# Performance work log

Measured on AMD Instinct MI355X. Metric: run time of the kernel, lower is better.

The kernel has to match this reference:

```python
import jax, jax.numpy as jnp
import numpy as np

SIZE = 1024
N_ITER = 10
TEMP = 0.125


def setup_inputs() -> dict:
    key = jax.random.key(0)
    k1, k2 = jax.random.split(key)
    x = jax.random.normal(k1, (8, 4096, SIZE), dtype=jnp.float32)
    # weight init: identity + small gaussian noise (matches torch init)
    weight = jnp.eye(SIZE, dtype=jnp.float32) + jax.random.normal(k2, (SIZE, SIZE), dtype=jnp.float32) * 1e-05
    return {"x": x, "weight": weight}


def _sinkhorn_project(weight):
    # log-space Sinkhorn normalization: n_iter steps of symmetric row/col
    # logsumexp subtraction, then exponentiate.
    log_P = weight / TEMP
    for _ in range(N_ITER):
        r_sum = jax.nn.logsumexp(log_P, axis=-1, keepdims=True)  # [size,1]
        c_sum = jax.nn.logsumexp(log_P, axis=-2, keepdims=True)  # [1,size]
        log_P = log_P - 0.5 * (r_sum + c_sum)
    return jnp.exp(log_P)


def reference(x, weight):
    W = _sinkhorn_project(weight)          # [size, size]
    # F.linear(x, W) == x @ W.T
    return jnp.einsum('bsd,od->bso', x, W)
```

## Files before the change

### kernel.cpp

```cpp
#include <hip/hip_runtime.h>
#include <hip/hip_bf16.h>


typedef __attribute__((ext_vector_type(8))) short short8;
typedef __attribute__((ext_vector_type(4))) float f32x4;

__device__ inline unsigned int pk2(float a, float b) {
  __hip_bfloat162 h = __float22bfloat162_rn(make_float2(a, b));
  union { __hip_bfloat162 h; unsigned int u; } cv;
  cv.h = h;
  return cv.u;
}

__global__ void sinkhorn_step(const float* __restrict__ w,
                              const float* __restrict__ Rin,
                              const float* __restrict__ Cin,
                              float* __restrict__ Rout,
                              float* __restrict__ Cout,
                              int first) {
  __shared__ float red[4];
  const int tid = threadIdx.x;
  const int b = blockIdx.x;
  const int lane = tid & 63, wv = tid >> 6;
  if (b < 1024) {
    const int j = tid * 4;
    float4 v = *(const float4*)(w + (size_t)b * 1024 + j);
    float4 cv = make_float4(0.f, 0.f, 0.f, 0.f);
    if (!first) cv = *(const float4*)(Cin + j);
    float s = __expf(8.f * v.x - 0.5f * cv.x) + __expf(8.f * v.y - 0.5f * cv.y)
            + __expf(8.f * v.z - 0.5f * cv.z) + __expf(8.f * v.w - 0.5f * cv.w);
    #pragma unroll
    for (int off = 32; off > 0; off >>= 1) s += __shfl_down(s, off);
    if (lane == 0) red[wv] = s;
    __syncthreads();
    if (tid == 0) {
      float t = red[0] + red[1] + red[2] + red[3];
      Rout[b] = (first ? 0.f : 0.5f * Rin[b]) + __logf(t);
    }
  } else {
    const int c = b - 1024;
    const int j = ((c & 7) << 7) + (c >> 3);
    const int i0 = tid * 4;
    const float* wp = w + (size_t)i0 * 1024 + j;
    float4 rv = make_float4(0.f, 0.f, 0.f, 0.f);
    if (!first) rv = *(const float4*)(Rin + i0);
    float s = __expf(8.f * wp[0]    - 0.5f * rv.x)
            + __expf(8.f * wp[1024] - 0.5f * rv.y)
            + __expf(8.f * wp[2048] - 0.5f * rv.z)
            + __expf(8.f * wp[3072] - 0.5f * rv.w);
    #pragma unroll
    for (int off = 32; off > 0; off >>= 1) s += __shfl_down(s, off);
    if (lane == 0) red[wv] = s;
    __syncthreads();
    if (tid == 0) {
      float t = red[0] + red[1] + red[2] + red[3];
      Cout[j] = (first ? 0.f : 0.5f * Cin[j]) + __logf(t);
    }
  }
}

__global__ void make_w(const float* __restrict__ w, const float* __restrict__ R,
                       const float* __restrict__ C, unsigned short* __restrict__ Wb) {
  const int i = blockIdx.x;
  const int j = threadIdx.x * 4;
  const float r = 0.5f * R[i];
  float4 v = *(const float4*)(w + (size_t)i * 1024 + j);
  float4 cv = *(const float4*)(C + j);
  unsigned int o[2];
  o[0] = pk2(__expf(8.f * v.x - r - 0.5f * cv.x), __expf(8.f * v.y - r - 0.5f * cv.y));
  o[1] = pk2(__expf(8.f * v.z - r - 0.5f * cv.z), __expf(8.f * v.w - r - 0.5f * cv.w));
  *(uint2*)(Wb + (size_t)i * 1024 + j) = *(uint2*)o;
}

__device__ inline void swizzle_mn(int id, int& m0, int& n0) {
  m0 = ((id & 7) + ((id >> 6) << 3)) << 7;
  n0 = ((id >> 3) & 7) << 7;
}

__global__ __launch_bounds__(256) void gemm_a(const float* __restrict__ X,
                                              const unsigned short* __restrict__ Wb,
                                              float* __restrict__ out) {
  __shared__ unsigned short As[128 * 32];
  __shared__ unsigned short Bs[128 * 32];
  const int tid = threadIdx.x;
  const int lane = tid & 63, wave = tid >> 6;
  const int wm = wave >> 1, wn = wave & 1;
  int m0, n0;
  swizzle_mn(blockIdx.x, m0, n0);

  f32x4 acc[4][4] = {};
  const int sr = tid >> 1, sk = (tid & 1) * 16;
  const float* Xrow = X + (size_t)(m0 + sr) * 1024 + sk;

  for (int k0 = 0; k0 < 1024; k0 += 32) {
    #pragma unroll
    for (int is = 0; is < 2; ++is) {
      int idx = is * 256 + tid;
      const unsigned short* g = Wb + (size_t)(n0 + (idx >> 2)) * 1024 + k0 + (idx & 3) * 8;
      unsigned short* l = Bs + (is * 256 + wave * 64) * 8;
      __builtin_amdgcn_global_load_lds(
          (const __attribute__((address_space(1))) unsigned int*)g,
          (__attribute__((address_space(3))) unsigned int*)l, 16, 0, 0);
    }
    float4 va0 = *(const float4*)(Xrow + k0);
    float4 va1 = *(const float4*)(Xrow + k0 + 4);
    float4 va2 = *(const float4*)(Xrow + k0 + 8);
    float4 va3 = *(const float4*)(Xrow + k0 + 12);
    unsigned int pk[8];
    pk[0] = pk2(va0.x, va0.y); pk[1] = pk2(va0.z, va0.w);
    pk[2] = pk2(va1.x, va1.y); pk[3] = pk2(va1.z, va1.w);
    pk[4] = pk2(va2.x, va2.y); pk[5] = pk2(va2.z, va2.w);
    pk[6] = pk2(va3.x, va3.y); pk[7] = pk2(va3.z, va3.w);
    *(uint4*)(As + sr * 32 + sk)     = *(uint4*)(pk);
    *(uint4*)(As + sr * 32 + sk + 8) = *(uint4*)(pk + 4);

    __syncthreads();

    const int kq = (lane >> 4) * 8;
    const int fr = lane & 15;
    short8 af[4], bf[4];
    #pragma unroll
    for (int t = 0; t < 4; ++t)
      af[t] = *(const short8*)(As + (wm * 64 + t * 16 + fr) * 32 + kq);
    #pragma unroll
    for (int t = 0; t < 4; ++t)
      bf[t] = *(const short8*)(Bs + (wn * 64 + t * 16 + fr) * 32 + kq);
    #pragma unroll
    for (int mt = 0; mt < 4; ++mt)
      #pragma unroll
      for (int nt = 0; nt < 4; ++nt)
        acc[mt][nt] = __builtin_amdgcn_mfma_f32_16x16x32_bf16(af[mt], bf[nt], acc[mt][nt], 0, 0, 0);

    __syncthreads();
  }

  const int crow0 = m0 + wm * 64 + (lane >> 4) * 4;
  const int ccol0 = n0 + wn * 64 + (lane & 15);
  #pragma unroll
  for (int mt = 0; mt < 4; ++mt)
    #pragma unroll
    for (int nt = 0; nt < 4; ++nt)
      #pragma unroll
      for (int r = 0; r < 4; ++r)
        out[(size_t)(crow0 + mt * 16 + r) * 1024 + ccol0 + nt * 16] = acc[mt][nt][r];
}

__global__ __launch_bounds__(256) void gemm_b(const float* __restrict__ X,
                                              const float* __restrict__ w,
                                              const float* __restrict__ R,
                                              const float* __restrict__ C,
                                              float* __restrict__ out) {
  __shared__ unsigned short As[128 * 32];
  __shared__ unsigned short Bs[128 * 32];
  const int tid = threadIdx.x;
  const int lane = tid & 63, wave = tid >> 6;
  const int wm = wave >> 1, wn = wave & 1;
  int m0, n0;
  swizzle_mn(blockIdx.x, m0, n0);

  f32x4 acc[4][4] = {};
  const int sr = tid >> 1, sk = (tid & 1) * 16;
  const float* Xrow = X + (size_t)(m0 + sr) * 1024 + sk;
  const float* Wrow = w + (size_t)(n0 + sr) * 1024 + sk;
  const float rpot = 0.5f * R[n0 + sr];

  for (int k0 = 0; k0 < 1024; k0 += 32) {
    float4 vb0 = *(const float4*)(Wrow + k0);
    float4 vb1 = *(const float4*)(Wrow + k0 + 4);
    float4 vb2 = *(const float4*)(Wrow + k0 + 8);
    float4 vb3 = *(const float4*)(Wrow + k0 + 12);
    float4 vc0 = *(const float4*)(C + k0 + sk);
    float4 vc1 = *(const float4*)(C + k0 + sk + 4);
    float4 vc2 = *(const float4*)(C + k0 + sk + 8);
    float4 vc3 = *(const float4*)(C + k0 + sk + 12);
    unsigned int pb[8];
    pb[0] = pk2(__expf(8.f * vb0.x - rpot - 0.5f * vc0.x), __expf(8.f * vb0.y - rpot - 0.5f * vc0.y));
    pb[1] = pk2(__expf(8.f * vb0.z - rpot - 0.5f * vc0.z), __expf(8.f * vb0.w - rpot - 0.5f * vc0.w));
    pb[2] = pk2(__expf(8.f * vb1.x - rpot - 0.5f * vc1.x), __expf(8.f * vb1.y - rpot - 0.5f * vc1.y));
    pb[3] = pk2(__expf(8.f * vb1.z - rpot - 0.5f * vc1.z), __expf(8.f * vb1.w - rpot - 0.5f * vc1.w));
    pb[4] = pk2(__expf(8.f * vb2.x - rpot - 0.5f * vc2.x), __expf(8.f * vb2.y - rpot - 0.5f * vc2.y));
    pb[5] = pk2(__expf(8.f * vb2.z - rpot - 0.5f * vc2.z), __expf(8.f * vb2.w - rpot - 0.5f * vc2.w));
    pb[6] = pk2(__expf(8.f * vb3.x - rpot - 0.5f * vc3.x), __expf(8.f * vb3.y - rpot - 0.5f * vc3.y));
    pb[7] = pk2(__expf(8.f * vb3.z - rpot - 0.5f * vc3.z), __expf(8.f * vb3.w - rpot - 0.5f * vc3.w));
    float4 va0 = *(const float4*)(Xrow + k0);
    float4 va1 = *(const float4*)(Xrow + k0 + 4);
    float4 va2 = *(const float4*)(Xrow + k0 + 8);
    float4 va3 = *(const float4*)(Xrow + k0 + 12);
    unsigned int pa[8];
    pa[0] = pk2(va0.x, va0.y); pa[1] = pk2(va0.z, va0.w);
    pa[2] = pk2(va1.x, va1.y); pa[3] = pk2(va1.z, va1.w);
    pa[4] = pk2(va2.x, va2.y); pa[5] = pk2(va2.z, va2.w);
    pa[6] = pk2(va3.x, va3.y); pa[7] = pk2(va3.z, va3.w);

    *(uint4*)(Bs + sr * 32 + sk)     = *(uint4*)(pb);
    *(uint4*)(Bs + sr * 32 + sk + 8) = *(uint4*)(pb + 4);
    *(uint4*)(As + sr * 32 + sk)     = *(uint4*)(pa);
    *(uint4*)(As + sr * 32 + sk + 8) = *(uint4*)(pa + 4);

    __syncthreads();

    const int kq = (lane >> 4) * 8;
    const int fr = lane & 15;
    short8 af[4], bf[4];
    #pragma unroll
    for (int t = 0; t < 4; ++t)
      af[t] = *(const short8*)(As + (wm * 64 + t * 16 + fr) * 32 + kq);
    #pragma unroll
    for (int t = 0; t < 4; ++t)
      bf[t] = *(const short8*)(Bs + (wn * 64 + t * 16 + fr) * 32 + kq);
    #pragma unroll
    for (int mt = 0; mt < 4; ++mt)
      #pragma unroll
      for (int nt = 0; nt < 4; ++nt)
        acc[mt][nt] = __builtin_amdgcn_mfma_f32_16x16x32_bf16(af[mt], bf[nt], acc[mt][nt], 0, 0, 0);

    __syncthreads();
  }

  const int crow0 = m0 + wm * 64 + (lane >> 4) * 4;
  const int ccol0 = n0 + wn * 64 + (lane & 15);
  #pragma unroll
  for (int mt = 0; mt < 4; ++mt)
    #pragma unroll
    for (int nt = 0; nt < 4; ++nt)
      #pragma unroll
      for (int r = 0; r < 4; ++r)
        out[(size_t)(crow0 + mt * 16 + r) * 1024 + ccol0 + nt * 16] = acc[mt][nt][r];
}

extern "C" void kernel_launch(void* const* d_in, const int* in_sizes, int n_in,
                              void* d_out, int out_size, void* d_ws, size_t ws_size,
                              hipStream_t stream) {
  const float* x = (const float*)d_in[0];
  const float* weight = (const float*)d_in[1];
  float* out = (float*)d_out;

  float* R0 = (float*)d_ws;
  float* C0 = R0 + 1024;
  float* R1 = C0 + 1024;
  float* C1 = R1 + 1024;
  unsigned short* Wb = (unsigned short*)(C1 + 1024);
  const size_t need_a = 16 * 1024 + 2 * 1024 * 1024;

  for (int t = 0; t < 10; ++t) {
    const float *Ri, *Ci;
    float *Ro, *Co;
    if ((t & 1) == 0) { Ri = R0; Ci = C0; Ro = R1; Co = C1; }
    else              { Ri = R1; Ci = C1; Ro = R0; Co = C0; }
    sinkhorn_step<<<2048, 256, 0, stream>>>(weight, Ri, Ci, Ro, Co, (t == 0) ? 1 : 0);
  }

  if (ws_size >= need_a) {
    make_w<<<1024, 256, 0, stream>>>(weight, R0, C0, Wb);
    gemm_a<<<2048, 256, 0, stream>>>(x, Wb, out);
  } else {
    gemm_b<<<2048, 256, 0, stream>>>(x, weight, R0, C0, out);
  }
}
```

Baseline: 394.0 us.

## Fuse Sinkhorn iterations into one cooperative kernel with grid barriers

Replaces the ten separate sinkhorn_step launches and the make_w launch with a single cooperative kernel of 256 blocks. Each block keeps its slice of exp(8w) in registers, both a row slice and a column slice, and iterates using multiplicative scaling vectors u and v, exchanged through global buffers and a hierarchical atomic grid barrier. This removes repeated launch overhead and repeated re-reading and re-exponentiating of the weight matrix on every iteration. The kernel then writes the bf16 projected weight directly for gemm_a. The trade-off is dependence on cooperative launch and on spin barriers, and it works in the linear domain instead of log space, which could lose precision.

```diff
diff --git a/kernel.cpp b/kernel.cpp
--- a/kernel.cpp
+++ b/kernel.cpp
@@ -10,6 +10,151 @@
   union { __hip_bfloat162 h; unsigned int u; } cv;
   cv.h = h;
   return cv.u;
+}
+
+__device__ __forceinline__ void gbarrier(int* bar, int it) {
+  __syncthreads();
+  if (threadIdx.x == 0) {
+    __threadfence();
+    int* subc = bar + it * 16 + (blockIdx.x & 15);
+    int a = __hip_atomic_fetch_add(subc, 1, __ATOMIC_ACQ_REL, __HIP_MEMORY_SCOPE_AGENT);
+    if (a == 15)
+      __hip_atomic_fetch_add(bar + 160 + it, 1, __ATOMIC_ACQ_REL, __HIP_MEMORY_SCOPE_AGENT);
+    int spins = 0;
+    while (__hip_atomic_load(bar + 160 + it, __ATOMIC_ACQUIRE, __HIP_MEMORY_SCOPE_AGENT) < 16) {
+      __builtin_amdgcn_s_sleep(8);
+      if (++spins > (1 << 22)) break;
+    }
+    __threadfence();
+  }
+  __syncthreads();
+}
+
+__global__ __launch_bounds__(256, 1) void sinkhorn_fused(
+    const float* __restrict__ w,
+    int* __restrict__ bar,
+    float* __restrict__ ubuf,
+    float* __restrict__ vbuf,
+    unsigned short* __restrict__ Wb) {
+  __shared__ float uL[1024];
+  __shared__ float vL[1024];
+  __shared__ float redC[4][4];
+  const int k = blockIdx.x;
+  const int t = threadIdx.x;
+  const int l = t & 63, wv = t >> 6;
+  const int row = 4 * k + wv;
+
+  float er[16];
+  {
+    const float* rp = w + (size_t)row * 1024 + l * 16;
+    #pragma unroll
+    for (int q = 0; q < 4; ++q) {
+      float4 v4 = *(const float4*)(rp + q * 4);
+      er[q * 4 + 0] = __expf(8.f * v4.x);
+      er[q * 4 + 1] = __expf(8.f * v4.y);
+      er[q * 4 + 2] = __expf(8.f * v4.z);
+      er[q * 4 + 3] = __expf(8.f * v4.w);
+    }
+  }
+  float ecs[4][4];
+  {
+    #pragma unroll
+    for (int q = 0; q < 4; ++q) {
+      float4 v4 = *(const float4*)(w + (size_t)(4 * t + q) * 1024 + 4 * k);
+      ecs[q][0] = __expf(8.f * v4.x);
+      ecs[q][1] = __expf(8.f * v4.y);
+      ecs[q][2] = __expf(8.f * v4.z);
+      ecs[q][3] = __expf(8.f * v4.w);
+    }
+  }
+
+  float vold = 1.f;
+  float uold = 1.f;
+
+  for (int it = 0; it < 10; ++it) {
+    const int rsl = it & 1;
+    const int wsl = (it + 1) & 1;
+    float ul[16], vv[4];
+    if (it == 0) {
+      #pragma unroll
+      for (int q = 0; q < 16; ++q) ul[q] = 1.f;
+      vv[0] = vv[1] = vv[2] = vv[3] = 1.f;
+    } else {
+      {
+        float4 uu = *(const float4*)(ubuf + rsl * 1024 + t * 4);
+        float4 vx = *(const float4*)(vbuf + rsl * 1024 + t * 4);
+        int cp = t ^ ((t >> 3) & 7);
+        *(float4*)(uL + cp * 4) = uu;
+        *(float4*)(vL + t * 4) = vx;
+      }
+      __syncthreads();
+      #pragma unroll
+      for (int q = 0; q < 4; ++q) {
+        int c = l * 4 + q;
+        int cp = c ^ ((c >> 3) & 7);
+        float4 u4 = *(const float4*)(uL + cp * 4);
+        ul[q * 4 + 0] = u4.x; ul[q * 4 + 1] = u4.y;
+        ul[q * 4 + 2] = u4.z; ul[q * 4 + 3] = u4.w;
+      }
+      float4 v4 = *(const float4*)(vL + t * 4);
+      vv[0] = v4.x; vv[1] = v4.y; vv[2] = v4.z; vv[3] = v4.w;
+    }
+
+    float rs = 0.f;
+    #pragma unroll
+    for (int q = 0; q < 16; ++q) rs += er[q] * ul[q];
+    #pragma unroll
+    for (int off = 32; off > 0; off >>= 1) rs += __shfl_down(rs, off);
+
+    float cs0 = 0.f, cs1 = 0.f, cs2 = 0.f, cs3 = 0.f;
+    #pragma unroll
+    for (int q = 0; q < 4; ++q) {
+      cs0 += ecs[q][0] * vv[q]; cs1 += ecs[q][1] * vv[q];
+      cs2 += ecs[q][2] * vv[q]; cs3 += ecs[q][3] * vv[q];
+    }
+    #pragma unroll
+    for (int off = 32; off > 0; off >>= 1) {
+      cs0 += __shfl_down(cs0, off); cs1 += __shfl_down(cs1, off);
+      cs2 += __shfl_down(cs2, off); cs3 += __shfl_down(cs3, off);
+    }
+    if (l == 0) {
+      redC[wv][0] = cs0; redC[wv][1] = cs1;
+      redC[wv][2] = cs2; redC[wv][3] = cs3;
+      vold = sqrtf(vold) * rsqrtf(rs);
+      vbuf[wsl * 1024 + row] = vold;
+    }
+    __syncthreads();
+    if (wv == 0 && l < 4) {
+      float tot = redC[0][l] + redC[1][l] + redC[2][l] + redC[3][l];
+      uold = sqrtf(uold) * rsqrtf(tot);
+      ubuf[wsl * 1024 + 4 * k + l] = uold;
+    }
+    gbarrier(bar, it);
+  }
+
+  {
+    float4 uu = *(const float4*)(ubuf + t * 4);
+    int cp = t ^ ((t >> 3) & 7);
+    *(float4*)(uL + cp * 4) = uu;
+  }
+  __syncthreads();
+  const float vfin = __shfl(vold, 0);
+  unsigned int o[8];
+  #pragma unroll
+  for (int q = 0; q < 4; ++q) {
+    int c = l * 4 + q;
+    int cp = c ^ ((c >> 3) & 7);
+    float4 u4 = *(const float4*)(uL + cp * 4);
+    float p0 = er[q * 4 + 0] * vfin * u4.x;
+    float p1 = er[q * 4 + 1] * vfin * u4.y;
+    float p2 = er[q * 4 + 2] * vfin * u4.z;
+    float p3 = er[q * 4 + 3] * vfin * u4.w;
+    o[q * 2 + 0] = pk2(p0, p1);
+    o[q * 2 + 1] = pk2(p2, p3);
+  }
+  unsigned short* wp = Wb + (size_t)row * 1024 + l * 16;
+  *(uint4*)(wp) = *(uint4*)(o);
+  *(uint4*)(wp + 8) = *(uint4*)(o + 4);
 }
 
 __global__ void sinkhorn_step(const float* __restrict__ w,
@@ -235,11 +380,39 @@
   const float* weight = (const float*)d_in[1];
   float* out = (float*)d_out;
 
+  int* bar = (int*)d_ws;
+  float* ubuf = (float*)d_ws + 256;
+  float* vbuf = ubuf + 2048;
+  unsigned short* WbP = (unsigned short*)(vbuf + 2048);
+  const size_t need_p = 1024 + 16 * 1024 + 2 * 1024 * 1024;
+
+  if (ws_size >= need_p) {
+    hipError_t e0 = hipMemsetAsync(bar, 0, 1024, stream);
+    if (e0 == hipSuccess) {
+      const float* warg = weight;
+      int* barArg = bar;
+      float* uArg = ubuf; float* vArg = vbuf;
+      unsigned short* WbArg = WbP;
+      void* args[5] = {(void*)&warg, (void*)&barArg, (void*)&uArg,
+                       (void*)&vArg, (void*)&WbArg};
+      hipError_t ce = hipLaunchCooperativeKernel((const void*)sinkhorn_fused,
+                                                 dim3(256), dim3(256), args, 0,
+                                                 stream);
+      if (ce == hipSuccess) {
+        gemm_a<<<2048, 256, 0, stream>>>(x, WbP, out);
+        return;
+      }
+      (void)hipGetLastError();
+    } else {
+      (void)hipGetLastError();
+    }
+  }
+
   float* R0 = (float*)d_ws;
   float* C0 = R0 + 1024;
   float* R1 = C0 + 1024;
   float* C1 = R1 + 1024;
-  unsigned short* Wb = (unsigned short*)(C1 + 1024);
+  unsigned short* Wb2 = (unsigned short*)(C1 + 1024);
   const size_t need_a = 16 * 1024 + 2 * 1024 * 1024;
 
   for (int t = 0; t < 10; ++t) {
@@ -249,10 +422,9 @@
     else              { Ri = R1; Ci = C1; Ro = R0; Co = C0; }
     sinkhorn_step<<<2048, 256, 0, stream>>>(weight, Ri, Ci, Ro, Co, (t == 0) ? 1 : 0);
   }
-
   if (ws_size >= need_a) {
-    make_w<<<1024, 256, 0, stream>>>(weight, R0, C0, Wb);
-    gemm_a<<<2048, 256, 0, stream>>>(x, Wb, out);
+    make_w<<<1024, 256, 0, stream>>>(weight, R0, C0, Wb2);
+    gemm_a<<<2048, 256, 0, stream>>>(x, Wb2, out);
   } else {
     gemm_b<<<2048, 256, 0, stream>>>(x, weight, R0, C0, out);
   }
```

Measured after the change: 554.2 us. +40.6%, slower.
